# Kernel tuning notes

Hardware: AMD Instinct MI355X
Metric: run time of the kernel (lower is better)

Reference implementation:

```python
import jax, jax.numpy as jnp
import numpy as np

B, S, D = 4, 2048, 1024
E, ES, K = 16, 256, 4  # n_experts, expert_size, top-k (= n_heads)
STD_GATE = 0.02


def setup_inputs() -> dict:
    key = jax.random.key(0)
    k1, k2, k3, k4 = jax.random.split(key, 4)
    x = jax.random.normal(k1, (B, S, D), dtype=jnp.float32)
    # init per module: gate ~ N(0, d^-0.5), keys ~ N(0, d^-0.5), values ~ N(0, size^-0.5)
    w_gate = jax.random.normal(k2, (E, D), dtype=jnp.float32) * (D ** -0.5)
    keys = jax.random.normal(k3, (E, D, ES), dtype=jnp.float32) * (D ** -0.5)
    values = jax.random.normal(k4, (E, ES, D), dtype=jnp.float32) * ((E * ES) ** -0.5)
    return {"x": x, "w_gate": w_gate, "keys": keys, "values": values}


def reference(x, w_gate, keys, values):
    # sigma-MoE forward (selection_mode='sigmoid', activation=relu,
    # num_selected = n_heads = K, no bias, no dropout, eval mode)
    xt = x.reshape(-1, D)                         # [T, D]
    T = xt.shape[0]
    logits = xt @ w_gate.T                        # [T, E]
    sel = jax.nn.sigmoid(logits)                  # sigmoid gating
    sel_val, sel_idx = jax.lax.top_k(sel, K)      # [T, K]
    # sparse gate weights as dense [T, E] mask (zeros for unselected experts)
    gate_w = jnp.zeros((T, E), dtype=x.dtype).at[
        jnp.arange(T)[:, None], sel_idx
    ].set(sel_val)
    # per-expert hidden: h[t,e,s] = relu(sum_d x[t,d] keys[e,d,s])
    h = jax.nn.relu(jnp.einsum('td,eds->tes', xt, keys))  # [T, E, ES]
    # weighted scatter back through values: out = sum_e gate * h_e @ values_e
    out = jnp.einsum('tes,te,esv->tv', h, gate_w, values)  # [T, D]
    return out.reshape(B, S, D)
```

## Files before the change

kernel.cpp:

```cpp
#include <hip/hip_runtime.h>
#include <hip/hip_bf16.h>
#include <stdint.h>

#define T_TOK 8192
#define DIM   1024
#define NEXP  16
#define ESZ   256
#define TOPK  4
#define BM    64
#define BK    64
#define NPAIR (T_TOK*TOPK)
#define NBLK  128
#define MAXROWS (NPAIR + NEXP*BM)
#define MAXTILES (NPAIR/BM + NEXP)

typedef __hip_bfloat16 bf16;
typedef short bf16x8 __attribute__((ext_vector_type(8)));
typedef float f32x4 __attribute__((ext_vector_type(4)));

__device__ __forceinline__ unsigned short f2bu(float f){
  __hip_bfloat16 b = __float2bfloat16(f);
  return *reinterpret_cast<unsigned short*>(&b);
}
__device__ __forceinline__ float bu2f(unsigned short u){
  __hip_bfloat16 b = *reinterpret_cast<__hip_bfloat16*>(&u);
  return __bfloat162float(b);
}

__device__ __forceinline__ void gload16(const void* g, void* l){
  __builtin_amdgcn_global_load_lds((const __attribute__((address_space(1))) void*)g,
                                   (__attribute__((address_space(3))) void*)l, 16, 0, 0);
}

__global__ __launch_bounds__(256) void k_gate_dot(const float* __restrict__ x,
    const float* __restrict__ wg, bf16* __restrict__ xb, float* __restrict__ plog)
{
  __shared__ float wlds[NEXP*512];
  const int tid = threadIdx.x;
  const int half = blockIdx.x & 1;
  const int tg   = blockIdx.x >> 1;

  {
    const float4* src = (const float4*)wg;
    float4* dst = (float4*)wlds;
#pragma unroll
    for (int i=0;i<8;i++){
      int idx = tid + i*256;
      int e = idx >> 7, d4 = idx & 127;
      dst[idx] = src[e*256 + half*128 + d4];
    }
  }
  __syncthreads();

  const int ts = tid >> 5;
  const int dc = tid & 31;
  const int t0 = tg*16 + ts, t1 = t0 + 8;
  const float* xr0 = x + (size_t)t0*DIM + half*512;
  const float* xr1 = x + (size_t)t1*DIM + half*512;
  unsigned short* xd0 = (unsigned short*)xb + (size_t)t0*DIM + half*512;
  unsigned short* xd1 = (unsigned short*)xb + (size_t)t1*DIM + half*512;

  float acc0[NEXP], acc1[NEXP];
#pragma unroll
  for (int e=0;e<NEXP;e++){ acc0[e]=0.f; acc1[e]=0.f; }

#pragma unroll
  for (int i=0;i<4;i++){
    const int d0 = i*128 + dc*4;
    float4 xv0 = *(const float4*)(xr0 + d0);
    float4 xv1 = *(const float4*)(xr1 + d0);
    ushort4 o0; o0.x=f2bu(xv0.x); o0.y=f2bu(xv0.y); o0.z=f2bu(xv0.z); o0.w=f2bu(xv0.w);
    ushort4 o1; o1.x=f2bu(xv1.x); o1.y=f2bu(xv1.y); o1.z=f2bu(xv1.z); o1.w=f2bu(xv1.w);
    *(ushort4*)(xd0 + d0) = o0;
    *(ushort4*)(xd1 + d0) = o1;
#pragma unroll
    for (int e=0;e<NEXP;e++){
      float4 w = *(const float4*)(wlds + e*512 + d0);
      acc0[e] += xv0.x*w.x + xv0.y*w.y + xv0.z*w.z + xv0.w*w.w;
      acc1[e] += xv1.x*w.x + xv1.y*w.y + xv1.z*w.z + xv1.w*w.w;
    }
  }

#pragma unroll
  for (int e=0;e<NEXP;e++){
#pragma unroll
    for (int s=1;s<32;s<<=1){
      acc0[e] += __shfl_xor(acc0[e], s);
      acc1[e] += __shfl_xor(acc1[e], s);
    }
  }

  if (dc==0){
    float* p0 = plog + (size_t)t0*32 + half*16;
    float* p1 = plog + (size_t)t1*32 + half*16;
#pragma unroll
    for (int i=0;i<4;i++){
      f32x4 v0 = {acc0[i*4],acc0[i*4+1],acc0[i*4+2],acc0[i*4+3]};
      f32x4 v1 = {acc1[i*4],acc1[i*4+1],acc1[i*4+2],acc1[i*4+3]};
      *(f32x4*)(p0 + i*4) = v0;
      *(f32x4*)(p1 + i*4) = v1;
    }
  }
}

__global__ __launch_bounds__(256) void k_gate_top4(const float* __restrict__ plog,
    int* __restrict__ sel_idx, float* __restrict__ sel_gate,
    int* __restrict__ block_hist)
{
  __shared__ int h[4][NEXP];
  const int tid = threadIdx.x;
  if (tid < 64) h[tid>>4][tid&15] = 0;
  __syncthreads();

  const int t = blockIdx.x*256 + tid;
  const float* p = plog + (size_t)t*32;
  float v[NEXP];
#pragma unroll
  for (int i=0;i<4;i++){
    f32x4 a = *(const f32x4*)(p + i*4);
    f32x4 b = *(const f32x4*)(p + 16 + i*4);
#pragma unroll
    for (int j=0;j<4;j++) v[i*4+j] = 1.f/(1.f + expf(-(a[j]+b[j])));
  }
#pragma unroll
  for (int k=0;k<TOPK;k++){
    float bv=-2.f; int bi=0;
#pragma unroll
    for (int e=0;e<NEXP;e++) if (v[e] > bv){ bv=v[e]; bi=e; }
    sel_idx[t*TOPK+k]=bi; sel_gate[t*TOPK+k]=bv;
    atomicAdd(&h[tid>>6][bi],1);
    v[bi] = -2.f;
  }
  __syncthreads();
  if (tid < 64)
    block_hist[((size_t)blockIdx.x*4 + (tid>>4))*NEXP + (tid&15)] = h[tid>>4][tid&15];
}

__global__ __launch_bounds__(256) void k_transpose2(const float* __restrict__ keys,
    const float* __restrict__ values, bf16* __restrict__ kT, bf16* __restrict__ vT)
{
  __shared__ float tile[32][33];
  const int which = blockIdx.y >> 4, e = blockIdx.y & 15;
  const int R = which ? ESZ : DIM, C = which ? DIM : ESZ;
  const float* src = (which ? values : keys) + (size_t)e*DIM*ESZ;
  bf16* dst = (which ? vT : kT) + (size_t)e*DIM*ESZ;
  const int ctiles = C/32;
  const int r0 = (blockIdx.x / ctiles)*32, c0 = (blockIdx.x % ctiles)*32;
  const int tx = threadIdx.x & 31, ty = threadIdx.x >> 5;
#pragma unroll
  for (int i=0;i<4;i++){ int r = ty + i*8; tile[r][tx] = src[(size_t)(r0+r)*C + c0 + tx]; }
  __syncthreads();
#pragma unroll
  for (int i=0;i<4;i++){ int r = ty + i*8; dst[(size_t)(c0+r)*R + r0 + tx] = __float2bfloat16(tile[tx][r]); }
}

__global__ void k_meta(const int* __restrict__ gh,
    int* __restrict__ tile_expert, int* __restrict__ tile_rowstart,
    int* __restrict__ tile_segend, int* __restrict__ block_base)
{
  __shared__ int sbc[NBLK][NEXP];
  __shared__ int cnt[NEXP], seg[NEXP];
  const int tid = threadIdx.x;
  for (int cell = tid; cell < NBLK*NEXP; cell += 256)
    sbc[cell>>4][cell&15] = gh[cell];
  __syncthreads();
  if (tid < NEXP){
    int s=0;
    for (int sb=0; sb<NBLK; sb++) s += sbc[sb][tid];
    cnt[tid]=s;
  }
  __syncthreads();
  if (tid==0){
    int off=0, tc=0;
    for (int e=0;e<NEXP;e++){
      seg[e]=off;
      int c = cnt[e];
      int nt = (c + BM - 1)/BM;
      for (int i=0;i<nt;i++){
        tile_expert[tc]=e; tile_rowstart[tc]=off+i*BM; tile_segend[tc]=off+c; tc++;
      }
      off += nt*BM;
    }
    for (; tc<MAXTILES; tc++) tile_expert[tc]=-1;
  }
  __syncthreads();
  if (tid < NEXP){
    int s = seg[tid];
    for (int sb=0; sb<NBLK; sb++){ block_base[sb*NEXP + tid] = s; s += sbc[sb][tid]; }
  }
}

__global__ __launch_bounds__(256) void k_scatter(const int* __restrict__ sel_idx,
    const float* __restrict__ sel_gate, const int* __restrict__ block_base,
    int* __restrict__ assign_pair, float* __restrict__ assign_gate)
{
  __shared__ int wcnt[4][NEXP];
  const int p = blockIdx.x*256 + threadIdx.x;
  const int wave = threadIdx.x >> 6, lane = threadIdx.x & 63;
  const int e = sel_idx[p];
  const float g = sel_gate[p];
  int rank = 0;
#pragma unroll
  for (int ee=0; ee<NEXP; ee++){
    unsigned long long m = __ballot(e==ee);
    if (lane==0) wcnt[wave][ee] = (int)__popcll(m);
    if (e==ee) rank = (int)__popcll(m & ((1ull<<lane)-1ull));
  }
  __syncthreads();
  int pre = 0;
  for (int w=0; w<wave; w++) pre += wcnt[w][e];
  const int row = block_base[blockIdx.x*NEXP + e] + pre + rank;
  assign_pair[row] = p;
  assign_gate[row] = g;
}

__global__ __launch_bounds__(256, 6) void k_gemm1(
    const bf16* __restrict__ xb, const bf16* __restrict__ kT,
    const int* __restrict__ assign_pair, const float* __restrict__ assign_gate,
    const int* __restrict__ tile_expert, const int* __restrict__ tile_rowstart,
    const int* __restrict__ tile_segend, bf16* __restrict__ h)
{
  __shared__ char smem[24576];
  __shared__ int   tokens_s[BM];
  __shared__ float gates_s[BM];

  const int nb = blockIdx.x, tile = blockIdx.y;
  const int e = tile_expert[tile];
  if (e < 0) return;
  const int row0 = tile_rowstart[tile];
  const int segend = tile_segend[tile];
  const int tid = threadIdx.x, wave = tid>>6, lane = tid&63;

  if (tid < BM){
    int rg = row0 + tid;
    bool vld = rg < segend;
    tokens_s[tid] = vld ? (assign_pair[rg] >> 2) : 0;
    gates_s[tid]  = vld ? assign_gate[rg] : 0.f;
  }
  __syncthreads();

  const bf16* qA[2]; const bf16* qB[4]; int loA[2], loB[4];
#pragma unroll
  for (int i=0;i<2;i++){
    int row = i*32 + wave*8 + (lane>>3);
    int c   = (lane&7) ^ (row&7);
    qA[i] = xb + (size_t)tokens_s[row]*DIM + c*8;
    loA[i] = i*4096 + wave*1024;
  }
#pragma unroll
  for (int i=0;i<4;i++){
    int col = i*32 + wave*8 + (lane>>3);
    int c   = (lane&7) ^ (col&7);
    qB[i] = kT + ((size_t)e*ESZ + nb*128 + col)*DIM + c*8;
    loB[i] = i*4096 + wave*1024;
  }

  const int wr0 = (wave>>1)*32, wc0 = (wave&1)*64;
  int offA[2][2], offB[2][4];
#pragma unroll
  for (int kk=0;kk<2;kk++){
    int kb = kk*64 + (lane>>4)*16;
#pragma unroll
    for (int m=0;m<2;m++){ int row = wr0 + m*16 + (lane&15); offA[kk][m] = row*128 + (kb ^ ((row&7)<<4)); }
#pragma unroll
    for (int n=0;n<4;n++){ int col = wc0 + n*16 + (lane&15); offB[kk][n] = col*128 + (kb ^ ((col&7)<<4)); }
  }

  f32x4 acc[2][4];
#pragma unroll
  for (int m=0;m<2;m++)
#pragma unroll
    for (int n=0;n<4;n++) acc[m][n] = {0.f,0.f,0.f,0.f};

  auto stage = [&](){
#pragma unroll
    for (int i=0;i<2;i++){ gload16(qA[i], smem + loA[i]); qA[i]+=BK; }
#pragma unroll
    for (int i=0;i<4;i++){ gload16(qB[i], smem + 8192 + loB[i]); qB[i]+=BK; }
  };
  auto compute = [&](){
#pragma unroll
    for (int kk=0;kk<2;kk++){
      bf16x8 af[2], bfr[4];
#pragma unroll
      for (int m=0;m<2;m++) af[m]  = *(const bf16x8*)(smem + offA[kk][m]);
#pragma unroll
      for (int n=0;n<4;n++) bfr[n] = *(const bf16x8*)(smem + 8192 + offB[kk][n]);
#pragma unroll
      for (int m=0;m<2;m++)
#pragma unroll
        for (int n=0;n<4;n++)
          acc[m][n] = __builtin_amdgcn_mfma_f32_16x16x32_bf16(af[m], bfr[n], acc[m][n], 0,0,0);
    }
  };

#pragma unroll 1
  for (int kt=0; kt<16; ++kt){
    stage();
    asm volatile("s_waitcnt vmcnt(0)" ::: "memory");
    __builtin_amdgcn_s_barrier();
    compute();
    __builtin_amdgcn_s_barrier();
  }

#pragma unroll
  for (int m=0;m<2;m++)
#pragma unroll
    for (int n=0;n<4;n++){
      int col = wc0 + n*16 + (lane&15);
#pragma unroll
      for (int j=0;j<4;j++){
        int rloc = wr0 + m*16 + ((lane>>4)<<2) + j;
        float v = fmaxf(acc[m][n][j], 0.f) * gates_s[rloc];
        h[(size_t)(row0 + rloc)*ESZ + nb*128 + col] = __float2bfloat16(v);
      }
    }
}

__global__ __launch_bounds__(256, 6) void k_gemm2(
    const bf16* __restrict__ h, const bf16* __restrict__ vT,
    const int* __restrict__ assign_pair,
    const int* __restrict__ tile_expert, const int* __restrict__ tile_rowstart,
    const int* __restrict__ tile_segend, bf16* __restrict__ partial)
{
  __shared__ char smem[24576];
  __shared__ int pairs_s[BM];

  const int nb = blockIdx.x, tile = blockIdx.y;
  const int e = tile_expert[tile];
  if (e < 0) return;
  const int row0 = tile_rowstart[tile];
  const int segend = tile_segend[tile];
  const int tid = threadIdx.x, wave = tid>>6, lane = tid&63;

  if (tid < BM){
    int rg = row0 + tid;
    pairs_s[tid] = (rg < segend) ? assign_pair[rg] : -1;
  }
  __syncthreads();

  const bf16* qA[2]; const bf16* qB[4]; int loA[2], loB[4];
#pragma unroll
  for (int i=0;i<2;i++){
    int row = i*32 + wave*8 + (lane>>3);
    int c   = (lane&7) ^ (row&7);
    qA[i] = h + (size_t)(row0 + row)*ESZ + c*8;
    loA[i] = i*4096 + wave*1024;
  }
#pragma unroll
  for (int i=0;i<4;i++){
    int col = i*32 + wave*8 + (lane>>3);
    int c   = (lane&7) ^ (col&7);
    qB[i] = vT + ((size_t)e*DIM + nb*128 + col)*ESZ + c*8;
    loB[i] = i*4096 + wave*1024;
  }

  const int wr0 = (wave>>1)*32, wc0 = (wave&1)*64;
  int offA[2][2], offB[2][4];
#pragma unroll
  for (int kk=0;kk<2;kk++){
    int kb = kk*64 + (lane>>4)*16;
#pragma unroll
    for (int m=0;m<2;m++){ int row = wr0 + m*16 + (lane&15); offA[kk][m] = row*128 + (kb ^ ((row&7)<<4)); }
#pragma unroll
    for (int n=0;n<4;n++){ int col = wc0 + n*16 + (lane&15); offB[kk][n] = col*128 + (kb ^ ((col&7)<<4)); }
  }

  f32x4 acc[2][4];
#pragma unroll
  for (int m=0;m<2;m++)
#pragma unroll
    for (int n=0;n<4;n++) acc[m][n] = {0.f,0.f,0.f,0.f};

  auto stage = [&](){
#pragma unroll
    for (int i=0;i<2;i++){ gload16(qA[i], smem + loA[i]); qA[i]+=BK; }
#pragma unroll
    for (int i=0;i<4;i++){ gload16(qB[i], smem + 8192 + loB[i]); qB[i]+=BK; }
  };
  auto compute = [&](){
#pragma unroll
    for (int kk=0;kk<2;kk++){
      bf16x8 af[2], bfr[4];
#pragma unroll
      for (int m=0;m<2;m++) af[m]  = *(const bf16x8*)(smem + offA[kk][m]);
#pragma unroll
      for (int n=0;n<4;n++) bfr[n] = *(const bf16x8*)(smem + 8192 + offB[kk][n]);
#pragma unroll
      for (int m=0;m<2;m++)
#pragma unroll
        for (int n=0;n<4;n++)
          acc[m][n] = __builtin_amdgcn_mfma_f32_16x16x32_bf16(af[m], bfr[n], acc[m][n], 0,0,0);
    }
  };

#pragma unroll 1
  for (int kt=0; kt<4; ++kt){
    stage();
    asm volatile("s_waitcnt vmcnt(0)" ::: "memory");
    __builtin_amdgcn_s_barrier();
    compute();
    __builtin_amdgcn_s_barrier();
  }

#pragma unroll
  for (int m=0;m<2;m++)
#pragma unroll
    for (int n=0;n<4;n++){
      int col = wc0 + n*16 + (lane&15);
#pragma unroll
      for (int j=0;j<4;j++){
        int rloc = wr0 + m*16 + ((lane>>4)<<2) + j;
        int pp = pairs_s[rloc];
        if (pp >= 0)
          partial[(size_t)pp*DIM + nb*128 + col] = __float2bfloat16(acc[m][n][j]);
      }
    }
}

__global__ __launch_bounds__(256) void k_reduce(const bf16* __restrict__ partial,
    float* __restrict__ out)
{
  const int tb = blockIdx.x*4;
  const int c0 = threadIdx.x * 4;
#pragma unroll
  for (int i=0;i<4;i++){
    const int t = tb + i;
    const unsigned short* pr = (const unsigned short*)partial + (size_t)t*4*DIM;
    float a0=0.f,a1=0.f,a2=0.f,a3=0.f;
#pragma unroll
    for (int k=0;k<TOPK;k++){
      ushort4 v = *(const ushort4*)(pr + k*DIM + c0);
      a0 += bu2f(v.x); a1 += bu2f(v.y); a2 += bu2f(v.z); a3 += bu2f(v.w);
    }
    float4 o = {a0,a1,a2,a3};
    *(float4*)(out + (size_t)t*DIM + c0) = o;
  }
}

extern "C" void kernel_launch(void* const* d_in, const int* in_sizes, int n_in,
                              void* d_out, int out_size, void* d_ws, size_t ws_size,
                              hipStream_t stream)
{
  const float* x      = (const float*)d_in[0];
  const float* wg     = (const float*)d_in[1];
  const float* keys   = (const float*)d_in[2];
  const float* values = (const float*)d_in[3];
  float* out = (float*)d_out;

  char* ws = (char*)d_ws;
  size_t off = 0;
  bf16* vT   = (bf16*)(ws+off); off += (size_t)NEXP*DIM*ESZ*2;
  bf16* hbuf = (bf16*)(ws+off); off += (size_t)MAXROWS*ESZ*2;
  float* plog         = (float*)(ws+off); off += (size_t)T_TOK*32*4;
  int*   sel_idx      = (int*)  (ws+off); off += (size_t)NPAIR*4;
  float* sel_gate     = (float*)(ws+off); off += (size_t)NPAIR*4;
  int*   assign_pair  = (int*)  (ws+off); off += (size_t)MAXROWS*4;
  float* assign_gate  = (float*)(ws+off); off += (size_t)MAXROWS*4;
  int*   block_hist   = (int*)  (ws+off); off += (size_t)NBLK*NEXP*4;
  int*   block_base   = (int*)  (ws+off); off += (size_t)NBLK*NEXP*4;
  int*   tile_expert  = (int*)  (ws+off); off += 4096;
  int*   tile_rowstart= (int*)  (ws+off); off += 4096;
  int*   tile_segend  = (int*)  (ws+off); off += 4096;
  const size_t PARTIAL_BYTES = (size_t)NPAIR*DIM*2;
  const size_t XB_BYTES = (size_t)T_TOK*DIM*2;
  const size_t KT_BYTES = (size_t)NEXP*ESZ*DIM*2;
  bf16* partial = (bf16*)(ws+off); off += PARTIAL_BYTES;
  bf16* xb = (bf16*)((char*)partial + PARTIAL_BYTES - XB_BYTES - KT_BYTES);
  bf16* kT = (bf16*)((char*)partial + PARTIAL_BYTES - KT_BYTES);

  k_gate_dot<<<T_TOK/16*2, 256, 0, stream>>>(x, wg, xb, plog);
  k_gate_top4<<<T_TOK/256, 256, 0, stream>>>(plog, sel_idx, sel_gate, block_hist);
  k_transpose2<<<dim3(256, NEXP*2), 256, 0, stream>>>(keys, values, kT, vT);
  k_meta<<<1, 256, 0, stream>>>(block_hist, tile_expert, tile_rowstart, tile_segend, block_base);
  k_scatter<<<NBLK, 256, 0, stream>>>(sel_idx, sel_gate, block_base, assign_pair, assign_gate);
  k_gemm1<<<dim3(2, MAXTILES), 256, 0, stream>>>(xb, kT, assign_pair, assign_gate,
      tile_expert, tile_rowstart, tile_segend, hbuf);
  k_gemm2<<<dim3(8, MAXTILES), 256, 0, stream>>>(hbuf, vT, assign_pair,
      tile_expert, tile_rowstart, tile_segend, partial);
  k_reduce<<<T_TOK/4, 256, 0, stream>>>(partial, out);
}
```

Baseline: 138.4 us.

## Process four tokens per thread in gate dot and pad segments to 128 rows

The gate-dot kernel now handles four tokens per thread instead of two, halving its grid and reusing each LDS weight load across more tokens. Expert segments are padded to 128-row tiles, and each GEMM block takes a 64-row half, skipping halves that start past the segment end. This cuts the number of blocks that exist only for tile bookkeeping, but can increase padding rows per expert and raises register pressure in the gate kernel.

```diff
diff --git a/kernel.cpp b/kernel.cpp
--- a/kernel.cpp
+++ b/kernel.cpp
@@ -7,12 +7,11 @@
 #define NEXP  16
 #define ESZ   256
 #define TOPK  4
-#define BM    64
 #define BK    64
 #define NPAIR (T_TOK*TOPK)
 #define NBLK  128
-#define MAXROWS (NPAIR + NEXP*BM)
-#define MAXTILES (NPAIR/BM + NEXP)
+#define MAXROWS (NPAIR + NEXP*128)
+#define MAXTILES (NPAIR/128 + NEXP)
 
 typedef __hip_bfloat16 bf16;
 typedef short bf16x8 __attribute__((ext_vector_type(8)));
@@ -54,30 +53,36 @@
 
   const int ts = tid >> 5;
   const int dc = tid & 31;
-  const int t0 = tg*16 + ts, t1 = t0 + 8;
-  const float* xr0 = x + (size_t)t0*DIM + half*512;
-  const float* xr1 = x + (size_t)t1*DIM + half*512;
-  unsigned short* xd0 = (unsigned short*)xb + (size_t)t0*DIM + half*512;
-  unsigned short* xd1 = (unsigned short*)xb + (size_t)t1*DIM + half*512;
-
-  float acc0[NEXP], acc1[NEXP];
-#pragma unroll
-  for (int e=0;e<NEXP;e++){ acc0[e]=0.f; acc1[e]=0.f; }
+  const int t0 = tg*32 + ts;
+  const float* xr[4]; unsigned short* xd[4];
+#pragma unroll
+  for (int q=0;q<4;q++){
+    xr[q] = x + (size_t)(t0+q*8)*DIM + half*512;
+    xd[q] = (unsigned short*)xb + (size_t)(t0+q*8)*DIM + half*512;
+  }
+
+  float acc[4][NEXP];
+#pragma unroll
+  for (int q=0;q<4;q++)
+#pragma unroll
+    for (int e=0;e<NEXP;e++) acc[q][e]=0.f;
 
 #pragma unroll
   for (int i=0;i<4;i++){
     const int d0 = i*128 + dc*4;
-    float4 xv0 = *(const float4*)(xr0 + d0);
-    float4 xv1 = *(const float4*)(xr1 + d0);
-    ushort4 o0; o0.x=f2bu(xv0.x); o0.y=f2bu(xv0.y); o0.z=f2bu(xv0.z); o0.w=f2bu(xv0.w);
-    ushort4 o1; o1.x=f2bu(xv1.x); o1.y=f2bu(xv1.y); o1.z=f2bu(xv1.z); o1.w=f2bu(xv1.w);
-    *(ushort4*)(xd0 + d0) = o0;
-    *(ushort4*)(xd1 + d0) = o1;
+    float4 xv[4];
+#pragma unroll
+    for (int q=0;q<4;q++){
+      xv[q] = *(const float4*)(xr[q] + d0);
+      ushort4 o; o.x=f2bu(xv[q].x); o.y=f2bu(xv[q].y); o.z=f2bu(xv[q].z); o.w=f2bu(xv[q].w);
+      *(ushort4*)(xd[q] + d0) = o;
+    }
 #pragma unroll
     for (int e=0;e<NEXP;e++){
       float4 w = *(const float4*)(wlds + e*512 + d0);
-      acc0[e] += xv0.x*w.x + xv0.y*w.y + xv0.z*w.z + xv0.w*w.w;
-      acc1[e] += xv1.x*w.x + xv1.y*w.y + xv1.z*w.z + xv1.w*w.w;
+#pragma unroll
+      for (int q=0;q<4;q++)
+        acc[q][e] += xv[q].x*w.x + xv[q].y*w.y + xv[q].z*w.z + xv[q].w*w.w;
     }
   }
 
@@ -85,20 +90,20 @@
   for (int e=0;e<NEXP;e++){
 #pragma unroll
     for (int s=1;s<32;s<<=1){
-      acc0[e] += __shfl_xor(acc0[e], s);
-      acc1[e] += __shfl_xor(acc1[e], s);
+#pragma unroll
+      for (int q=0;q<4;q++) acc[q][e] += __shfl_xor(acc[q][e], s);
     }
   }
 
   if (dc==0){
-    float* p0 = plog + (size_t)t0*32 + half*16;
-    float* p1 = plog + (size_t)t1*32 + half*16;
-#pragma unroll
-    for (int i=0;i<4;i++){
-      f32x4 v0 = {acc0[i*4],acc0[i*4+1],acc0[i*4+2],acc0[i*4+3]};
-      f32x4 v1 = {acc1[i*4],acc1[i*4+1],acc1[i*4+2],acc1[i*4+3]};
-      *(f32x4*)(p0 + i*4) = v0;
-      *(f32x4*)(p1 + i*4) = v1;
+#pragma unroll
+    for (int q=0;q<4;q++){
+      float* p = plog + (size_t)(t0+q*8)*32 + half*16;
+#pragma unroll
+      for (int i=0;i<4;i++){
+        f32x4 v = {acc[q][i*4],acc[q][i*4+1],acc[q][i*4+2],acc[q][i*4+3]};
+        *(f32x4*)(p + i*4) = v;
+      }
     }
   }
 }
@@ -175,11 +180,11 @@
     for (int e=0;e<NEXP;e++){
       seg[e]=off;
       int c = cnt[e];
-      int nt = (c + BM - 1)/BM;
+      int nt = (c + 127)/128;
       for (int i=0;i<nt;i++){
-        tile_expert[tc]=e; tile_rowstart[tc]=off+i*BM; tile_segend[tc]=off+c; tc++;
+        tile_expert[tc]=e; tile_rowstart[tc]=off+i*128; tile_segend[tc]=off+c; tc++;
       }
-      off += nt*BM;
+      off += nt*128;
     }
     for (; tc<MAXTILES; tc++) tile_expert[tc]=-1;
   }
@@ -221,17 +226,18 @@
     const int* __restrict__ tile_segend, bf16* __restrict__ h)
 {
   __shared__ char smem[24576];
-  __shared__ int   tokens_s[BM];
-  __shared__ float gates_s[BM];
-
-  const int nb = blockIdx.x, tile = blockIdx.y;
+  __shared__ int   tokens_s[64];
+  __shared__ float gates_s[64];
+
+  const int nb = blockIdx.x, tile = blockIdx.y >> 1, half = blockIdx.y & 1;
   const int e = tile_expert[tile];
   if (e < 0) return;
-  const int row0 = tile_rowstart[tile];
+  const int row0 = tile_rowstart[tile] + half*64;
   const int segend = tile_segend[tile];
+  if (row0 >= segend) return;
   const int tid = threadIdx.x, wave = tid>>6, lane = tid&63;
 
-  if (tid < BM){
+  if (tid < 64){
     int rg = row0 + tid;
     bool vld = rg < segend;
     tokens_s[tid] = vld ? (assign_pair[rg] >> 2) : 0;
@@ -324,16 +330,17 @@
     const int* __restrict__ tile_segend, bf16* __restrict__ partial)
 {
   __shared__ char smem[24576];
-  __shared__ int pairs_s[BM];
-
-  const int nb = blockIdx.x, tile = blockIdx.y;
+  __shared__ int pairs_s[64];
+
+  const int nb = blockIdx.x, tile = blockIdx.y >> 1, half = blockIdx.y & 1;
   const int e = tile_expert[tile];
   if (e < 0) return;
-  const int row0 = tile_rowstart[tile];
+  const int row0 = tile_rowstart[tile] + half*64;
   const int segend = tile_segend[tile];
+  if (row0 >= segend) return;
   const int tid = threadIdx.x, wave = tid>>6, lane = tid&63;
 
-  if (tid < BM){
+  if (tid < 64){
     int rg = row0 + tid;
     pairs_s[tid] = (rg < segend) ? assign_pair[rg] : -1;
   }
@@ -469,14 +476,14 @@
   bf16* xb = (bf16*)((char*)partial + PARTIAL_BYTES - XB_BYTES - KT_BYTES);
   bf16* kT = (bf16*)((char*)partial + PARTIAL_BYTES - KT_BYTES);
 
-  k_gate_dot<<<T_TOK/16*2, 256, 0, stream>>>(x, wg, xb, plog);
+  k_gate_dot<<<T_TOK/32*2, 256, 0, stream>>>(x, wg, xb, plog);
   k_gate_top4<<<T_TOK/256, 256, 0, stream>>>(plog, sel_idx, sel_gate, block_hist);
   k_transpose2<<<dim3(256, NEXP*2), 256, 0, stream>>>(keys, values, kT, vT);
   k_meta<<<1, 256, 0, stream>>>(block_hist, tile_expert, tile_rowstart, tile_segend, block_base);
   k_scatter<<<NBLK, 256, 0, stream>>>(sel_idx, sel_gate, block_base, assign_pair, assign_gate);
-  k_gemm1<<<dim3(2, MAXTILES), 256, 0, stream>>>(xb, kT, assign_pair, assign_gate,
+  k_gemm1<<<dim3(2, MAXTILES*2), 256, 0, stream>>>(xb, kT, assign_pair, assign_gate,
       tile_expert, tile_rowstart, tile_segend, hbuf);
-  k_gemm2<<<dim3(8, MAXTILES), 256, 0, stream>>>(hbuf, vT, assign_pair,
+  k_gemm2<<<dim3(8, MAXTILES*2), 256, 0, stream>>>(hbuf, vT, assign_pair,
       tile_expert, tile_rowstart, tile_segend, partial);
   k_reduce<<<T_TOK/4, 256, 0, stream>>>(partial, out);
 }
```

Result: no change. 137.6 us (-0.5%).
